# Performance work log

Hardware: AMD Instinct MI355X
Metric: run time of the kernel (lower is better)

## Reference

```python
import jax, jax.numpy as jnp
import numpy as np

WINDOW = 48
RES = 50
PRED = 96

def setup_inputs() -> dict:
    key = jax.random.key(0)
    k1, k2, k3, k4, k5 = jax.random.split(key, 5)
    x = jax.random.normal(k1, (2048, 4800, 1), dtype=jnp.float32)
    W_lin = jax.random.normal(k2, (WINDOW, WINDOW), dtype=jnp.float32) * 0.1
    # W_in = inv(P) @ B with P orthogonal, B ~ U(-1,1); statistically a dense random matrix
    W_in = jax.random.uniform(k3, (RES, WINDOW), dtype=jnp.float32, minval=-1.0, maxval=1.0)
    # diagonal reservoir weights d ~ U(-0.95, 0.95)
    d = jax.random.uniform(k4, (RES,), dtype=jnp.float32, minval=-0.95, maxval=0.95)
    W_out = jax.random.normal(k5, (PRED, RES), dtype=jnp.float32) * 0.1
    return {"x": x, "W_lin": W_lin, "W_in": W_in, "d": d, "W_out": W_out}

def reference(x, W_lin, W_in, d, W_out):
    B, S, C = x.shape  # C == 1 (non-individual path requires squeeze(1))
    seg = S // WINDOW
    # permute(0,2,1) -> view(B, C, seg, WINDOW) -> squeeze(1)
    u = x[..., 0].reshape(B, seg, WINDOW)
    # input linear (no bias): u @ W_lin.T
    u = jnp.einsum('bsw,vw->bsv', u, W_lin)
    # input projection into reservoir: W_in @ u_t for every step (one big GEMM)
    v = jnp.einsum('bsw,rw->bsr', u, W_in)  # [B, seg, RES]
    # ESN state persists across the batch loop too (never reset in update_state),
    # so the recurrence is one serial chain over B*seg steps.
    v_flat = v.reshape(B * seg, RES)
    def step(state, vt):
        # activation is LeakyReLU(negative_slope=1.0) == identity
        new = vt + d * state
        return new, new
    _, states = jax.lax.scan(step, jnp.zeros((RES,), dtype=v.dtype), v_flat)
    states = states.reshape(B, seg, RES)
    last = states[:, -1, :]              # [B, RES]
    out = last @ W_out.T                 # [B, PRED]
    return out[:, :, None]               # unsqueeze(1).permute(0,2,1) -> [B, PRED, 1]
```

## Files before the change

kernel.cpp:

```cpp
#include <hip/hip_runtime.h>

#define WINDOW 48
#define RES 50
#define PRED 96
#define BATCH 2048
#define KTOT 4800
#define KPAD 5120
#define KTRUNC 12
#define KS 30
#define KRB 160

typedef __attribute__((ext_vector_type(8))) short short8v;
typedef __attribute__((ext_vector_type(4))) float f32x4;

#define OFF_DK 0
#define OFF_WT 800
#define OFF_KB 5600
#define OFF_LP 169440

__device__ __forceinline__ float ipow(float b, int n) {
    float r = 1.f, p = b;
    while (n) { if (n & 1) r *= p; p *= p; n >>= 1; }
    return r;
}

__global__ __launch_bounds__(256) void k0(const float* __restrict__ W_lin,
                                          const float* __restrict__ W_in,
                                          const float* __restrict__ d,
                                          const float* __restrict__ W_out,
                                          float* __restrict__ ws) {
    unsigned f = blockIdx.x * 256 + threadIdx.x;
    if (f < 800) {
        int k = f / RES, r = f % RES;
        ws[OFF_DK + f] = ipow(ipow(d[r], 100), k);
    } else if (f < 5600) {
        int e = f - 800;
        int r = e / PRED, o = e % PRED;
        ws[OFF_WT + e] = W_out[o * RES + r];
    }
    if (f < 64u * KPAD) {
        int c = f / KPAD, k = f - (f / KPAD) * KPAD;
        float val = 0.f;
        if (c < RES && k < KTOT) {
            int j = k / WINDOW, w = k - j * WINDOW;
            float m = 0.f;
            for (int v = 0; v < WINDOW; ++v)
                m = fmaf(W_in[c * WINDOW + v], W_lin[v * WINDOW + w], m);
            val = ipow(d[c], 99 - j) * m;
        }
        unsigned u = __builtin_bit_cast(unsigned, val);
        ((unsigned short*)(ws + OFF_KB))[f] =
            (unsigned short)((u + 0x7FFFu + ((u >> 16) & 1u)) >> 16);
    }
}

#define LOADA(st, A0, A1) { A0 = *(const f32x4*)(ap + (st) * 32); \
                            A1 = *(const f32x4*)(ap + (st) * 32 + 4); }
#define LOADB(st, B0, B1, B2, B3) { const unsigned short* p_ = bp + (st) * 32; \
    B0 = *(const short8v*)p_;                    B1 = *(const short8v*)(p_ + 16 * KPAD); \
    B2 = *(const short8v*)(p_ + 32 * KPAD);      B3 = *(const short8v*)(p_ + 48 * KPAD); }
#define COMPUTE(A0, A1, B0, B1, B2, B3) { \
    short8v ahi, alo; \
    _Pragma("unroll") \
    for (int m_ = 0; m_ < 8; ++m_) { \
        float v_ = (m_ < 4) ? A0[m_] : A1[m_ - 4]; \
        unsigned u_ = __builtin_bit_cast(unsigned, v_); \
        unsigned hb_ = (u_ + 0x7FFFu + ((u_ >> 16) & 1u)) & 0xFFFF0000u; \
        ahi[m_] = (short)(hb_ >> 16); \
        float r_ = v_ - __builtin_bit_cast(float, hb_); \
        unsigned u2_ = __builtin_bit_cast(unsigned, r_); \
        alo[m_] = (short)((u2_ + 0x7FFFu + ((u2_ >> 16) & 1u)) >> 16); \
    } \
    acc0 = __builtin_amdgcn_mfma_f32_16x16x32_bf16(ahi, B0, acc0, 0, 0, 0); \
    acc0 = __builtin_amdgcn_mfma_f32_16x16x32_bf16(alo, B0, acc0, 0, 0, 0); \
    acc1 = __builtin_amdgcn_mfma_f32_16x16x32_bf16(ahi, B1, acc1, 0, 0, 0); \
    acc1 = __builtin_amdgcn_mfma_f32_16x16x32_bf16(alo, B1, acc1, 0, 0, 0); \
    acc2 = __builtin_amdgcn_mfma_f32_16x16x32_bf16(ahi, B2, acc2, 0, 0, 0); \
    acc2 = __builtin_amdgcn_mfma_f32_16x16x32_bf16(alo, B2, acc2, 0, 0, 0); \
    acc3 = __builtin_amdgcn_mfma_f32_16x16x32_bf16(ahi, B3, acc3, 0, 0, 0); \
    acc3 = __builtin_amdgcn_mfma_f32_16x16x32_bf16(alo, B3, acc3, 0, 0, 0); }

__global__ __launch_bounds__(128, 4) void k1p(const float* __restrict__ x,
                                              const float* __restrict__ ws,
                                              float* __restrict__ lp) {
    const unsigned short* Kb = (const unsigned short*)(ws + OFF_KB);
    int bid = blockIdx.x;
    int mt = bid / 15, sg = bid - mt * 15;
    int t = threadIdx.x;
    int w = t >> 6, l = t & 63;
    int s = sg * 2 + w;
    int b0 = mt * 16;
    int row16 = l & 15, kq = l >> 4;
    int kw = s * KRB + kq * 8;

    const float* ap = x + (size_t)(b0 + row16) * KTOT + kw;
    const unsigned short* bp = Kb + (size_t)row16 * KPAD + kw;

    f32x4 acc0 = (f32x4)(0.f), acc1 = (f32x4)(0.f), acc2 = (f32x4)(0.f), acc3 = (f32x4)(0.f);

    f32x4 a0s0, a1s0, a0s1, a1s1, a0s2, a1s2;
    short8v b0s0, b1s0, b2s0, b3s0, b0s1, b1s1, b2s1, b3s1, b0s2, b1s2, b2s2, b3s2;

    LOADA(0, a0s0, a1s0) LOADB(0, b0s0, b1s0, b2s0, b3s0)
    LOADA(1, a0s1, a1s1) LOADB(1, b0s1, b1s1, b2s1, b3s1)
    LOADA(2, a0s2, a1s2) LOADB(2, b0s2, b1s2, b2s2, b3s2)

    COMPUTE(a0s0, a1s0, b0s0, b1s0, b2s0, b3s0)
    LOADA(3, a0s0, a1s0) LOADB(3, b0s0, b1s0, b2s0, b3s0)
    COMPUTE(a0s1, a1s1, b0s1, b1s1, b2s1, b3s1)
    LOADA(4, a0s1, a1s1) LOADB(4, b0s1, b1s1, b2s1, b3s1)
    COMPUTE(a0s2, a1s2, b0s2, b1s2, b2s2, b3s2)
    COMPUTE(a0s0, a1s0, b0s0, b1s0, b2s0, b3s0)
    COMPUTE(a0s1, a1s1, b0s1, b1s1, b2s1, b3s1)

    float* dst = lp + ((size_t)s * BATCH + b0) * 50;
#pragma unroll
    for (int i = 0; i < 4; ++i) {
        int r = kq * 4 + i;
        dst[(size_t)r * 50 + row16]      = acc0[i];
        dst[(size_t)r * 50 + row16 + 16] = acc1[i];
        dst[(size_t)r * 50 + row16 + 32] = acc2[i];
        if (row16 < 2) dst[(size_t)r * 50 + row16 + 48] = acc3[i];
    }
}

__global__ __launch_bounds__(256) void k2(const float* __restrict__ ws,
                                          float* __restrict__ out) {
    __shared__ float Ls[27 * 52];
    __shared__ float Ss[16 * 52];
    const float* lp = ws + OFF_LP;
    const float* Dk = ws + OFF_DK;
    const float* Wt = ws + OFF_WT;
    int B0 = blockIdx.x * 16;
    int t = threadIdx.x;

    for (int e = t; e < 27 * 50; e += 256) {
        int lr = e / 50, c = e - lr * 50;
        int bb = B0 - 11 + lr;
        float sum = 0.f;
        if (bb >= 0) {
#pragma unroll
            for (int sp = 0; sp < KS; ++sp)
                sum += lp[((size_t)sp * BATCH + bb) * 50 + c];
        }
        Ls[lr * 52 + c] = sum;
    }
    __syncthreads();

    for (int e = t; e < 16 * 50; e += 256) {
        int i = e / 50, r = e - i * 50;
        float acc = 0.f;
#pragma unroll
        for (int k = 0; k < KTRUNC; ++k)
            acc = fmaf(Dk[k * RES + r], Ls[(11 + i - k) * 52 + r], acc);
        Ss[i * 52 + r] = acc;
    }
    __syncthreads();

    for (int e = t; e < 16 * PRED; e += 256) {
        int i = e / PRED, o = e - i * PRED;
        float acc = 0.f;
#pragma unroll 10
        for (int r = 0; r < RES; ++r)
            acc = fmaf(Ss[i * 52 + r], Wt[r * PRED + o], acc);
        out[(B0 + i) * PRED + o] = acc;
    }
}

extern "C" void kernel_launch(void* const* d_in, const int* in_sizes, int n_in,
                              void* d_out, int out_size, void* d_ws, size_t ws_size,
                              hipStream_t stream) {
    const float* x     = (const float*)d_in[0];
    const float* W_lin = (const float*)d_in[1];
    const float* W_in  = (const float*)d_in[2];
    const float* d     = (const float*)d_in[3];
    const float* W_out = (const float*)d_in[4];
    float* out = (float*)d_out;
    float* ws  = (float*)d_ws;
    float* lp  = ws + OFF_LP;

    k0<<<1280, 256, 0, stream>>>(W_lin, W_in, d, W_out, ws);
    k1p<<<128 * 15, 128, 0, stream>>>(x, ws, lp);
    k2<<<128, 256, 0, stream>>>(ws, out);
}
```

Baseline: 41.03 us.

## Use single bf16 pass for x, retile K-split, hoist W_in·W_lin product

The main GEMM now rounds x to bf16 once instead of splitting it into hi and lo bf16 parts. This halves the MFMA count and drops most of the conversion ALU work, at the cost of lower accuracy on x. The K dimension is re-split into 20 chunks of 256 using 256-thread blocks with a deeper load pipeline, and out-of-range A loads are redirected to a safe address. The setup kernel computes the W_in·W_lin product once per block in shared memory rather than once per output element, and runs with far fewer blocks.

New measurement: 55.65 us. 35.6% more time.

```diff
diff --git a/kernel.cpp b/kernel.cpp
--- a/kernel.cpp
+++ b/kernel.cpp
@@ -7,11 +7,12 @@
 #define KTOT 4800
 #define KPAD 5120
 #define KTRUNC 12
-#define KS 30
-#define KRB 160
+#define KS 20
+#define KRB 256
 
 typedef __attribute__((ext_vector_type(8))) short short8v;
 typedef __attribute__((ext_vector_type(4))) float f32x4;
+typedef __attribute__((ext_vector_type(4))) int i32x4;
 
 #define OFF_DK 0
 #define OFF_WT 800
@@ -24,12 +25,22 @@
     return r;
 }
 
+__device__ __forceinline__ unsigned pack2bf(float v0, float v1) {
+    unsigned u0 = __builtin_bit_cast(unsigned, v0);
+    unsigned u1 = __builtin_bit_cast(unsigned, v1);
+    unsigned t0 = u0 + 0x7FFFu + ((u0 >> 16) & 1u);
+    unsigned t1 = u1 + 0x7FFFu + ((u1 >> 16) & 1u);
+    return (t0 >> 16) | (t1 & 0xFFFF0000u);
+}
+
 __global__ __launch_bounds__(256) void k0(const float* __restrict__ W_lin,
                                           const float* __restrict__ W_in,
                                           const float* __restrict__ d,
                                           const float* __restrict__ W_out,
                                           float* __restrict__ ws) {
-    unsigned f = blockIdx.x * 256 + threadIdx.x;
+    __shared__ float Ml[RES * WINDOW];
+    int t = threadIdx.x, bid = blockIdx.x;
+    int f = bid * 256 + t;
     if (f < 800) {
         int k = f / RES, r = f % RES;
         ws[OFF_DK + f] = ipow(ipow(d[r], 100), k);
@@ -38,57 +49,57 @@
         int r = e / PRED, o = e % PRED;
         ws[OFF_WT + e] = W_out[o * RES + r];
     }
-    if (f < 64u * KPAD) {
-        int c = f / KPAD, k = f - (f / KPAD) * KPAD;
+    for (int e = t; e < RES * WINDOW; e += 256) {
+        int c = e / WINDOW, w = e - c * WINDOW;
+        float acc = 0.f;
+        for (int v = 0; v < WINDOW; ++v)
+            acc = fmaf(W_in[c * WINDOW + v], W_lin[v * WINDOW + w], acc);
+        Ml[e] = acc;
+    }
+    __syncthreads();
+    unsigned short* Kb = (unsigned short*)(ws + OFF_KB);
+    unsigned base = bid * 2560u;
+#pragma unroll
+    for (int i = 0; i < 10; ++i) {
+        unsigned e = base + t + i * 256;
+        int c = e / KPAD, k = e - (e / KPAD) * KPAD;
         float val = 0.f;
         if (c < RES && k < KTOT) {
             int j = k / WINDOW, w = k - j * WINDOW;
-            float m = 0.f;
-            for (int v = 0; v < WINDOW; ++v)
-                m = fmaf(W_in[c * WINDOW + v], W_lin[v * WINDOW + w], m);
-            val = ipow(d[c], 99 - j) * m;
+            val = ipow(d[c], 99 - j) * Ml[c * WINDOW + w];
         }
         unsigned u = __builtin_bit_cast(unsigned, val);
-        ((unsigned short*)(ws + OFF_KB))[f] =
-            (unsigned short)((u + 0x7FFFu + ((u >> 16) & 1u)) >> 16);
+        Kb[e] = (unsigned short)((u + 0x7FFFu + ((u >> 16) & 1u)) >> 16);
     }
 }
 
-#define LOADA(st, A0, A1) { A0 = *(const f32x4*)(ap + (st) * 32); \
-                            A1 = *(const f32x4*)(ap + (st) * 32 + 4); }
-#define LOADB(st, B0, B1, B2, B3) { const unsigned short* p_ = bp + (st) * 32; \
-    B0 = *(const short8v*)p_;                    B1 = *(const short8v*)(p_ + 16 * KPAD); \
-    B2 = *(const short8v*)(p_ + 32 * KPAD);      B3 = *(const short8v*)(p_ + 48 * KPAD); }
-#define COMPUTE(A0, A1, B0, B1, B2, B3) { \
-    short8v ahi, alo; \
-    _Pragma("unroll") \
-    for (int m_ = 0; m_ < 8; ++m_) { \
-        float v_ = (m_ < 4) ? A0[m_] : A1[m_ - 4]; \
-        unsigned u_ = __builtin_bit_cast(unsigned, v_); \
-        unsigned hb_ = (u_ + 0x7FFFu + ((u_ >> 16) & 1u)) & 0xFFFF0000u; \
-        ahi[m_] = (short)(hb_ >> 16); \
-        float r_ = v_ - __builtin_bit_cast(float, hb_); \
-        unsigned u2_ = __builtin_bit_cast(unsigned, r_); \
-        alo[m_] = (short)((u2_ + 0x7FFFu + ((u2_ >> 16) & 1u)) >> 16); \
-    } \
-    acc0 = __builtin_amdgcn_mfma_f32_16x16x32_bf16(ahi, B0, acc0, 0, 0, 0); \
-    acc0 = __builtin_amdgcn_mfma_f32_16x16x32_bf16(alo, B0, acc0, 0, 0, 0); \
-    acc1 = __builtin_amdgcn_mfma_f32_16x16x32_bf16(ahi, B1, acc1, 0, 0, 0); \
-    acc1 = __builtin_amdgcn_mfma_f32_16x16x32_bf16(alo, B1, acc1, 0, 0, 0); \
-    acc2 = __builtin_amdgcn_mfma_f32_16x16x32_bf16(ahi, B2, acc2, 0, 0, 0); \
-    acc2 = __builtin_amdgcn_mfma_f32_16x16x32_bf16(alo, B2, acc2, 0, 0, 0); \
-    acc3 = __builtin_amdgcn_mfma_f32_16x16x32_bf16(ahi, B3, acc3, 0, 0, 0); \
-    acc3 = __builtin_amdgcn_mfma_f32_16x16x32_bf16(alo, B3, acc3, 0, 0, 0); }
+#define LOADA(st, A0, A1) {                                                   \
+    const float* p_ = (kw + (st) * 32 < KTOT) ? (ap + (st) * 32) : x;         \
+    A0 = *(const f32x4*)p_;  A1 = *(const f32x4*)(p_ + 4); }
+#define LOADB(st, B0, B1, B2, B3) {                                           \
+    const unsigned short* p_ = bp + (st) * 32;                                \
+    B0 = *(const short8v*)p_;                B1 = *(const short8v*)(p_ + 16 * KPAD); \
+    B2 = *(const short8v*)(p_ + 32 * KPAD);  B3 = *(const short8v*)(p_ + 48 * KPAD); }
+#define COMPUTE(A0, A1, B0, B1, B2, B3) {                                     \
+    i32x4 wv;                                                                 \
+    wv[0] = (int)pack2bf(A0[0], A0[1]);                                       \
+    wv[1] = (int)pack2bf(A0[2], A0[3]);                                       \
+    wv[2] = (int)pack2bf(A1[0], A1[1]);                                       \
+    wv[3] = (int)pack2bf(A1[2], A1[3]);                                       \
+    short8v av = __builtin_bit_cast(short8v, wv);                             \
+    acc0 = __builtin_amdgcn_mfma_f32_16x16x32_bf16(av, B0, acc0, 0, 0, 0);    \
+    acc1 = __builtin_amdgcn_mfma_f32_16x16x32_bf16(av, B1, acc1, 0, 0, 0);    \
+    acc2 = __builtin_amdgcn_mfma_f32_16x16x32_bf16(av, B2, acc2, 0, 0, 0);    \
+    acc3 = __builtin_amdgcn_mfma_f32_16x16x32_bf16(av, B3, acc3, 0, 0, 0); }
 
-__global__ __launch_bounds__(128, 4) void k1p(const float* __restrict__ x,
-                                              const float* __restrict__ ws,
-                                              float* __restrict__ lp) {
+__global__ __launch_bounds__(256, 3) void k1(const float* __restrict__ x,
+                                             const float* __restrict__ ws,
+                                             float* __restrict__ lp) {
     const unsigned short* Kb = (const unsigned short*)(ws + OFF_KB);
     int bid = blockIdx.x;
-    int mt = bid / 15, sg = bid - mt * 15;
-    int t = threadIdx.x;
-    int w = t >> 6, l = t & 63;
-    int s = sg * 2 + w;
+    int mt = bid / 5, sg = bid - mt * 5;
+    int t = threadIdx.x, w = t >> 6, l = t & 63;
+    int s = sg * 4 + w;
     int b0 = mt * 16;
     int row16 = l & 15, kq = l >> 4;
     int kw = s * KRB + kq * 8;
@@ -98,20 +109,21 @@
 
     f32x4 acc0 = (f32x4)(0.f), acc1 = (f32x4)(0.f), acc2 = (f32x4)(0.f), acc3 = (f32x4)(0.f);
 
-    f32x4 a0s0, a1s0, a0s1, a1s1, a0s2, a1s2;
-    short8v b0s0, b1s0, b2s0, b3s0, b0s1, b1s1, b2s1, b3s1, b0s2, b1s2, b2s2, b3s2;
+    f32x4 a0p, a1p, a0q, a1q, a0r, a1r;
+    short8v b0p, b1p, b2p, b3p, b0q, b1q, b2q, b3q, b0r, b1r, b2r, b3r;
 
-    LOADA(0, a0s0, a1s0) LOADB(0, b0s0, b1s0, b2s0, b3s0)
-    LOADA(1, a0s1, a1s1) LOADB(1, b0s1, b1s1, b2s1, b3s1)
-    LOADA(2, a0s2, a1s2) LOADB(2, b0s2, b1s2, b2s2, b3s2)
+    LOADA(0, a0p, a1p) LOADB(0, b0p, b1p, b2p, b3p)
+    LOADA(1, a0q, a1q) LOADB(1, b0q, b1q, b2q, b3q)
+    LOADA(2, a0r, a1r) LOADB(2, b0r, b1r, b2r, b3r)
 
-    COMPUTE(a0s0, a1s0, b0s0, b1s0, b2s0, b3s0)
-    LOADA(3, a0s0, a1s0) LOADB(3, b0s0, b1s0, b2s0, b3s0)
-    COMPUTE(a0s1, a1s1, b0s1, b1s1, b2s1, b3s1)
-    LOADA(4, a0s1, a1s1) LOADB(4, b0s1, b1s1, b2s1, b3s1)
-    COMPUTE(a0s2, a1s2, b0s2, b1s2, b2s2, b3s2)
-    COMPUTE(a0s0, a1s0, b0s0, b1s0, b2s0, b3s0)
-    COMPUTE(a0s1, a1s1, b0s1, b1s1, b2s1, b3s1)
+    COMPUTE(a0p, a1p, b0p, b1p, b2p, b3p)  LOADA(3, a0p, a1p) LOADB(3, b0p, b1p, b2p, b3p)
+    COMPUTE(a0q, a1q, b0q, b1q, b2q, b3q)  LOADA(4, a0q, a1q) LOADB(4, b0q, b1q, b2q, b3q)
+    COMPUTE(a0r, a1r, b0r, b1r, b2r, b3r)  LOADA(5, a0r, a1r) LOADB(5, b0r, b1r, b2r, b3r)
+    COMPUTE(a0p, a1p, b0p, b1p, b2p, b3p)  LOADA(6, a0p, a1p) LOADB(6, b0p, b1p, b2p, b3p)
+    COMPUTE(a0q, a1q, b0q, b1q, b2q, b3q)  LOADA(7, a0q, a1q) LOADB(7, b0q, b1q, b2q, b3q)
+    COMPUTE(a0r, a1r, b0r, b1r, b2r, b3r)
+    COMPUTE(a0p, a1p, b0p, b1p, b2p, b3p)
+    COMPUTE(a0q, a1q, b0q, b1q, b2q, b3q)
 
     float* dst = lp + ((size_t)s * BATCH + b0) * 50;
 #pragma unroll
@@ -179,7 +191,7 @@
     float* ws  = (float*)d_ws;
     float* lp  = ws + OFF_LP;
 
-    k0<<<1280, 256, 0, stream>>>(W_lin, W_in, d, W_out, ws);
-    k1p<<<128 * 15, 128, 0, stream>>>(x, ws, lp);
+    k0<<<128, 256, 0, stream>>>(W_lin, W_in, d, W_out, ws);
+    k1<<<640, 256, 0, stream>>>(x, ws, lp);
     k2<<<128, 256, 0, stream>>>(ws, out);
 }
```
